# Optimization experiments

Hardware: AMD Instinct MI355X
Metric: run time of the kernel (lower is better)

## Reference

```python
import jax, jax.numpy as jnp
import numpy as np

# Model dims (Gemma-class)
B, T, HID = 1, 3072, 2048
H, KH, D = 16, 8, 128          # q heads, kv heads, head_dim
WIN = 1024                     # sliding window
EPS = 1e-6
SEQ = 1536                     # two packed sequences of length 1536


def _rms(x, w):
    # torch nn.RMSNorm: x * rsqrt(mean(x^2) + eps) [* weight]
    var = jnp.mean(x * x, axis=-1, keepdims=True)
    y = x * jax.lax.rsqrt(var + EPS)
    return y if w is None else y * w


def _rotate_half(x):
    x1, x2 = jnp.split(x, 2, axis=-1)
    return jnp.concatenate([-x2, x1], axis=-1)


def _rope(x, cos, sin):
    # x: [B,T,h,D]; cos/sin: [B,T,rd] -> unsqueeze head dim (matches cos.unsqueeze(2))
    c = cos[:, :, None, :]
    s = sin[:, :, None, :]
    rd = cos.shape[-1]
    xr, xp = x[..., :rd], x[..., rd:]
    xr = xr * c + _rotate_half(xr) * s
    return jnp.concatenate([xr, xp], axis=-1)


def _build_mask(cu_seqlens):
    # causal & within sliding window & same packed sequence (matches _sliding_mask)
    idx = jnp.arange(T)
    seg = jnp.searchsorted(cu_seqlens, idx, side='right') - 1
    i = idx[:, None]
    j = idx[None, :]
    return (i >= j) & ((i - j) < WIN) & (seg[:, None] == seg[None, :])


def _attn_layer(x, wq, qn, k, v, wo, cos, sin, mask):
    # x: [B,T,HID]; k,v: [T,KH,D] (possibly shared from an earlier layer)
    q = _rope(_rms((x @ wq).reshape(B, T, H, D), qn), cos, sin).reshape(T, H, D)
    rep = H // k.shape[1]
    kk = jnp.repeat(k, rep, axis=1)   # GQA: repeat_interleave over head dim
    vv = jnp.repeat(v, rep, axis=1)
    s = jnp.einsum('qhd,khd->hqk', q, kk)          # scale = 1.0 (as in source)
    s = jnp.where(mask, s, jnp.asarray(-1e30, s.dtype))
    p = jax.nn.softmax(s, axis=-1)
    o = jnp.einsum('hqk,khd->qhd', p, vv).reshape(B, T, H * D)
    return o @ wo


def setup_inputs() -> dict:
    key = jax.random.key(0)
    ks = jax.random.split(key, 10)
    hidden_states = jax.random.normal(ks[0], (B, T, HID), jnp.float32)
    # RoPE tables with per-packed-sequence position resets
    pos = jnp.concatenate([jnp.arange(SEQ), jnp.arange(SEQ)]).astype(jnp.float32)
    inv = 1.0 / (10000.0 ** (jnp.arange(0, D, 2, dtype=jnp.float32) / D))
    fr = pos[:, None] * inv[None, :]
    emb = jnp.concatenate([fr, fr], axis=-1)     # [T, D]
    cos = jnp.cos(emb)[None]                     # [1, T, D]
    sin = jnp.sin(emb)[None]
    w = lambda k, sh: 0.02 * jax.random.normal(k, sh, jnp.float32)
    return {
        'hidden_states': hidden_states,
        'cos': cos, 'sin': sin,
        'wq0': w(ks[1], (HID, H * D)), 'wk0': w(ks[2], (HID, KH * D)),
        'wv0': w(ks[3], (HID, KH * D)), 'wo0': w(ks[4], (H * D, HID)),
        'qn0': 1.0 + 0.01 * jax.random.normal(ks[5], (D,), jnp.float32),
        'kn0': 1.0 + 0.01 * jax.random.normal(ks[6], (D,), jnp.float32),
        'wq1': w(ks[7], (HID, H * D)), 'wo1': w(ks[8], (H * D, HID)),
        'qn1': 1.0 + 0.01 * jax.random.normal(ks[9], (D,), jnp.float32),
        'cu_seqlens': jnp.array([0, SEQ, T], dtype=jnp.int32),
    }


def reference(hidden_states, cos, sin, wq0, wk0, wv0, wo0, qn0, kn0, wq1, wo1, qn1, cu_seqlens):
    mask = _build_mask(cu_seqlens)
    # Layer 0: source layer -> computes and stores K/V
    k = _rope(_rms((hidden_states @ wk0).reshape(B, T, KH, D), kn0), cos, sin).reshape(T, KH, D)
    v = _rms((hidden_states @ wv0).reshape(B, T, KH, D), None).reshape(T, KH, D)
    out0 = _attn_layer(hidden_states, wq0, qn0, k, v, wo0, cos, sin, mask)
    # Layer 1: KV-shared layer -> reuses layer 0's K/V (skips k/v projections)
    out1 = _attn_layer(out0, wq1, qn1, k, v, wo1, cos, sin, mask)
    return out1
```

## Files before the change

### kernel.cpp

```cpp
#include <hip/hip_runtime.h>
#include <hip/hip_bf16.h>

#define T_TOK 3072
#define HIDDEN 2048
#define NHQ 16
#define NHKV 8
#define DH 128
#define WINDOW 1024

typedef __attribute__((ext_vector_type(4))) float f32x4;
typedef __attribute__((ext_vector_type(8))) short bf16x8;
typedef __attribute__((ext_vector_type(8))) unsigned short ushort8;
typedef __attribute__((ext_vector_type(4))) unsigned short ushort4v;

__device__ __forceinline__ unsigned short f2bf(float f) {
  union { float fv; unsigned u; } v; v.fv = f;
  unsigned r = v.u + 0x7fffu + ((v.u >> 16) & 1u);
  return (unsigned short)(r >> 16);
}
__device__ __forceinline__ float bf2f(unsigned short h) {
  union { unsigned u; float f; } v; v.u = ((unsigned)h) << 16;
  return v.f;
}
__device__ __forceinline__ void split2(float f, unsigned short& hi, unsigned short& lo) {
  hi = f2bf(f);
  lo = f2bf(f - bf2f(hi));
}

__global__ __launch_bounds__(256) void cvt_split(const float* __restrict__ x,
                                                 unsigned short* __restrict__ yh,
                                                 unsigned short* __restrict__ yl, int n) {
  int i = (blockIdx.x * 256 + threadIdx.x) * 4;
  if (i >= n) return;
  f32x4 v = *(const f32x4*)(x + i);
  ushort4v oh, ol;
#pragma unroll
  for (int j = 0; j < 4; ++j) {
    unsigned short h, l;
    split2(v[j], h, l);
    oh[j] = h; ol[j] = l;
  }
  *(ushort4v*)(yh + i) = oh;
  *(ushort4v*)(yl + i) = ol;
}

__global__ __launch_bounds__(256) void transpose_w_split(const float* __restrict__ W,
                                                         unsigned short* __restrict__ Wth,
                                                         unsigned short* __restrict__ Wtl,
                                                         int K, int N) {
  __shared__ float tile[32][33];
  int bn = blockIdx.x * 32, bk = blockIdx.y * 32;
  int tx = threadIdx.x & 31, ty = threadIdx.x >> 5;
#pragma unroll
  for (int i = 0; i < 4; ++i)
    tile[ty + i * 8][tx] = W[(size_t)(bk + ty + i * 8) * N + bn + tx];
  __syncthreads();
#pragma unroll
  for (int i = 0; i < 4; ++i) {
    unsigned short h, l;
    split2(tile[tx][ty + i * 8], h, l);
    Wth[(size_t)(bn + ty + i * 8) * K + bk + tx] = h;
    if (Wtl) Wtl[(size_t)(bn + ty + i * 8) * K + bk + tx] = l;
  }
}

__global__ __launch_bounds__(256) void transpose_u16(const unsigned short* __restrict__ src,
                                                     unsigned short* __restrict__ dst,
                                                     int R, int C) {
  __shared__ unsigned short tile[32][33];
  int bc = blockIdx.x * 32, br = blockIdx.y * 32;
  int tx = threadIdx.x & 31, ty = threadIdx.x >> 5;
#pragma unroll
  for (int i = 0; i < 4; ++i)
    tile[ty + i * 8][tx] = src[(size_t)(br + ty + i * 8) * C + bc + tx];
  __syncthreads();
#pragma unroll
  for (int i = 0; i < 4; ++i)
    dst[(size_t)(bc + ty + i * 8) * R + br + tx] = tile[tx][ty + i * 8];
}

__global__ __launch_bounds__(256) void gemm3_128(const unsigned short* __restrict__ Ah,
                                                 const unsigned short* __restrict__ Al,
                                                 const unsigned short* __restrict__ Bh,
                                                 const unsigned short* __restrict__ Bl,
                                                 float* __restrict__ Cq,
                                                 float* __restrict__ Ckv,
                                                 int strd, int M, int N, int K) {
  __shared__ unsigned short ah_lds[128 * 32];
  __shared__ unsigned short al_lds[128 * 32];
  __shared__ unsigned short bh_lds[128 * 32];
  __shared__ unsigned short bl_lds[128 * 32];
  const int tid = threadIdx.x, lane = tid & 63, wave = tid >> 6;
  const int wr = (wave >> 1) * 64, wc = (wave & 1) * 64;
  const int g = lane >> 4, r16 = lane & 15;
  int nwg = gridDim.x * gridDim.y;
  int id = blockIdx.y * gridDim.x + blockIdx.x;
  int nid = (id & 7) * (nwg >> 3) + (id >> 3);
  const int bm = nid % gridDim.x, bn = nid / gridDim.x;
  f32x4 acc[4][4];
#pragma unroll
  for (int i = 0; i < 4; ++i)
#pragma unroll
    for (int j = 0; j < 4; ++j) acc[i][j] = (f32x4){0.f, 0.f, 0.f, 0.f};

  const unsigned short* AhB = Ah + (size_t)bm * 128 * K;
  const unsigned short* AlB = Al + (size_t)bm * 128 * K;
  const unsigned short* BhB = Bh + (size_t)bn * 128 * K;
  const unsigned short* BlB = Bl + (size_t)bn * 128 * K;

  for (int kt = 0; kt < K; kt += 32) {
    __syncthreads();
#pragma unroll
    for (int c = 0; c < 2; ++c) {
      size_t goff = (size_t)(wave * 32 + c * 16 + (lane >> 2)) * K + kt + (lane & 3) * 8;
      int loff = (wave * 2 + c) * 512;
      __builtin_amdgcn_global_load_lds(
          (const __attribute__((address_space(1))) unsigned int*)(AhB + goff),
          (__attribute__((address_space(3))) unsigned int*)(ah_lds + loff), 16, 0, 0);
      __builtin_amdgcn_global_load_lds(
          (const __attribute__((address_space(1))) unsigned int*)(AlB + goff),
          (__attribute__((address_space(3))) unsigned int*)(al_lds + loff), 16, 0, 0);
      __builtin_amdgcn_global_load_lds(
          (const __attribute__((address_space(1))) unsigned int*)(BhB + goff),
          (__attribute__((address_space(3))) unsigned int*)(bh_lds + loff), 16, 0, 0);
      __builtin_amdgcn_global_load_lds(
          (const __attribute__((address_space(1))) unsigned int*)(BlB + goff),
          (__attribute__((address_space(3))) unsigned int*)(bl_lds + loff), 16, 0, 0);
    }
    __syncthreads();
    bf16x8 ahf[4], alf[4], bhf[4], blf[4];
#pragma unroll
    for (int i = 0; i < 4; ++i) {
      ahf[i] = *(const bf16x8*)&ah_lds[(wr + i * 16 + r16) * 32 + g * 8];
      alf[i] = *(const bf16x8*)&al_lds[(wr + i * 16 + r16) * 32 + g * 8];
      bhf[i] = *(const bf16x8*)&bh_lds[(wc + i * 16 + r16) * 32 + g * 8];
      blf[i] = *(const bf16x8*)&bl_lds[(wc + i * 16 + r16) * 32 + g * 8];
    }
#pragma unroll
    for (int i = 0; i < 4; ++i)
#pragma unroll
      for (int j = 0; j < 4; ++j) {
        acc[i][j] = __builtin_amdgcn_mfma_f32_16x16x32_bf16(ahf[i], bhf[j], acc[i][j], 0, 0, 0);
        acc[i][j] = __builtin_amdgcn_mfma_f32_16x16x32_bf16(ahf[i], blf[j], acc[i][j], 0, 0, 0);
        acc[i][j] = __builtin_amdgcn_mfma_f32_16x16x32_bf16(alf[i], bhf[j], acc[i][j], 0, 0, 0);
      }
  }

#pragma unroll
  for (int i = 0; i < 4; ++i) {
    int row = bm * 128 + wr + i * 16 + g * 4;
#pragma unroll
    for (int j = 0; j < 4; ++j) {
      int colg = bn * 128 + wc + j * 16 + r16;
      float* Cb; int cc;
      if (colg < 2048) { Cb = Cq; cc = colg; } else { Cb = Ckv; cc = colg - 2048; }
#pragma unroll
      for (int r = 0; r < 4; ++r)
        Cb[(size_t)(row + r) * strd + cc] = acc[i][j][r];
    }
  }
}

template <int OUT>
__global__ __launch_bounds__(256) void gemm3_96(const unsigned short* __restrict__ Ah,
                                                const unsigned short* __restrict__ Al,
                                                const unsigned short* __restrict__ Bh,
                                                const unsigned short* __restrict__ Bl,
                                                float* __restrict__ Cf,
                                                unsigned short* __restrict__ Ch,
                                                unsigned short* __restrict__ Cl,
                                                int M, int N, int K) {
  __shared__ unsigned short ah_lds[96 * 32];
  __shared__ unsigned short al_lds[96 * 32];
  __shared__ unsigned short bh_lds[128 * 32];
  __shared__ unsigned short bl_lds[128 * 32];
  const int tid = threadIdx.x, lane = tid & 63, wave = tid >> 6;
  const int wr = (wave >> 1) * 48, wc = (wave & 1) * 64;
  const int g = lane >> 4, r16 = lane & 15;
  int nwg = gridDim.x * gridDim.y;
  int id = blockIdx.y * gridDim.x + blockIdx.x;
  int nid = (id & 7) * (nwg >> 3) + (id >> 3);
  const int bm = nid % gridDim.x, bn = nid / gridDim.x;
  f32x4 acc[3][4];
#pragma unroll
  for (int i = 0; i < 3; ++i)
#pragma unroll
    for (int j = 0; j < 4; ++j) acc[i][j] = (f32x4){0.f, 0.f, 0.f, 0.f};

  const unsigned short* AhB = Ah + (size_t)bm * 96 * K;
  const unsigned short* AlB = Al + (size_t)bm * 96 * K;
  const unsigned short* BhB = Bh + (size_t)bn * 128 * K;
  const unsigned short* BlB = Bl + (size_t)bn * 128 * K;

  for (int kt = 0; kt < K; kt += 32) {
    __syncthreads();
    {
      int c = wave;
      size_t goff = (size_t)(c * 16 + (lane >> 2)) * K + kt + (lane & 3) * 8;
      __builtin_amdgcn_global_load_lds(
          (const __attribute__((address_space(1))) unsigned int*)(AhB + goff),
          (__attribute__((address_space(3))) unsigned int*)(ah_lds + c * 512), 16, 0, 0);
      __builtin_amdgcn_global_load_lds(
          (const __attribute__((address_space(1))) unsigned int*)(AlB + goff),
          (__attribute__((address_space(3))) unsigned int*)(al_lds + c * 512), 16, 0, 0);
      if (wave < 2) {
        int c2 = 4 + wave;
        size_t goff2 = (size_t)(c2 * 16 + (lane >> 2)) * K + kt + (lane & 3) * 8;
        __builtin_amdgcn_global_load_lds(
            (const __attribute__((address_space(1))) unsigned int*)(AhB + goff2),
            (__attribute__((address_space(3))) unsigned int*)(ah_lds + c2 * 512), 16, 0, 0);
        __builtin_amdgcn_global_load_lds(
            (const __attribute__((address_space(1))) unsigned int*)(AlB + goff2),
            (__attribute__((address_space(3))) unsigned int*)(al_lds + c2 * 512), 16, 0, 0);
      }
    }
#pragma unroll
    for (int c = 0; c < 2; ++c) {
      size_t goff = (size_t)(wave * 32 + c * 16 + (lane >> 2)) * K + kt + (lane & 3) * 8;
      int loff = (wave * 2 + c) * 512;
      __builtin_amdgcn_global_load_lds(
          (const __attribute__((address_space(1))) unsigned int*)(BhB + goff),
          (__attribute__((address_space(3))) unsigned int*)(bh_lds + loff), 16, 0, 0);
      __builtin_amdgcn_global_load_lds(
          (const __attribute__((address_space(1))) unsigned int*)(BlB + goff),
          (__attribute__((address_space(3))) unsigned int*)(bl_lds + loff), 16, 0, 0);
    }
    __syncthreads();
    bf16x8 ahf[3], alf[3], bhf[4], blf[4];
#pragma unroll
    for (int i = 0; i < 3; ++i) {
      ahf[i] = *(const bf16x8*)&ah_lds[(wr + i * 16 + r16) * 32 + g * 8];
      alf[i] = *(const bf16x8*)&al_lds[(wr + i * 16 + r16) * 32 + g * 8];
    }
#pragma unroll
    for (int j = 0; j < 4; ++j) {
      bhf[j] = *(const bf16x8*)&bh_lds[(wc + j * 16 + r16) * 32 + g * 8];
      blf[j] = *(const bf16x8*)&bl_lds[(wc + j * 16 + r16) * 32 + g * 8];
    }
#pragma unroll
    for (int i = 0; i < 3; ++i)
#pragma unroll
      for (int j = 0; j < 4; ++j) {
        acc[i][j] = __builtin_amdgcn_mfma_f32_16x16x32_bf16(ahf[i], bhf[j], acc[i][j], 0, 0, 0);
        acc[i][j] = __builtin_amdgcn_mfma_f32_16x16x32_bf16(ahf[i], blf[j], acc[i][j], 0, 0, 0);
        acc[i][j] = __builtin_amdgcn_mfma_f32_16x16x32_bf16(alf[i], bhf[j], acc[i][j], 0, 0, 0);
      }
  }

#pragma unroll
  for (int i = 0; i < 3; ++i) {
    int row = bm * 96 + wr + i * 16 + g * 4;
#pragma unroll
    for (int j = 0; j < 4; ++j) {
      int col = bn * 128 + wc + j * 16 + r16;
#pragma unroll
      for (int r = 0; r < 4; ++r) {
        if (OUT == 0) {
          Cf[(size_t)(row + r) * N + col] = acc[i][j][r];
        } else {
          unsigned short h, l;
          split2(acc[i][j][r], h, l);
          Ch[(size_t)(row + r) * N + col] = h;
          Cl[(size_t)(row + r) * N + col] = l;
        }
      }
    }
  }
}

__global__ __launch_bounds__(256) void gemm1_96(const unsigned short* __restrict__ Ah,
                                                const unsigned short* __restrict__ Bh,
                                                float* __restrict__ Cf,
                                                int M, int N, int K) {
  __shared__ unsigned short ah_lds[96 * 32];
  __shared__ unsigned short bh_lds[128 * 32];
  const int tid = threadIdx.x, lane = tid & 63, wave = tid >> 6;
  const int wr = (wave >> 1) * 48, wc = (wave & 1) * 64;
  const int g = lane >> 4, r16 = lane & 15;
  int nwg = gridDim.x * gridDim.y;
  int id = blockIdx.y * gridDim.x + blockIdx.x;
  int nid = (id & 7) * (nwg >> 3) + (id >> 3);
  const int bm = nid % gridDim.x, bn = nid / gridDim.x;
  f32x4 acc[3][4];
#pragma unroll
  for (int i = 0; i < 3; ++i)
#pragma unroll
    for (int j = 0; j < 4; ++j) acc[i][j] = (f32x4){0.f, 0.f, 0.f, 0.f};

  const unsigned short* AhB = Ah + (size_t)bm * 96 * K;
  const unsigned short* BhB = Bh + (size_t)bn * 128 * K;

  for (int kt = 0; kt < K; kt += 32) {
    __syncthreads();
    {
      int c = wave;
      size_t goff = (size_t)(c * 16 + (lane >> 2)) * K + kt + (lane & 3) * 8;
      __builtin_amdgcn_global_load_lds(
          (const __attribute__((address_space(1))) unsigned int*)(AhB + goff),
          (__attribute__((address_space(3))) unsigned int*)(ah_lds + c * 512), 16, 0, 0);
      if (wave < 2) {
        int c2 = 4 + wave;
        size_t goff2 = (size_t)(c2 * 16 + (lane >> 2)) * K + kt + (lane & 3) * 8;
        __builtin_amdgcn_global_load_lds(
            (const __attribute__((address_space(1))) unsigned int*)(AhB + goff2),
            (__attribute__((address_space(3))) unsigned int*)(ah_lds + c2 * 512), 16, 0, 0);
      }
    }
#pragma unroll
    for (int c = 0; c < 2; ++c) {
      size_t goff = (size_t)(wave * 32 + c * 16 + (lane >> 2)) * K + kt + (lane & 3) * 8;
      __builtin_amdgcn_global_load_lds(
          (const __attribute__((address_space(1))) unsigned int*)(BhB + goff),
          (__attribute__((address_space(3))) unsigned int*)(bh_lds + (wave * 2 + c) * 512), 16, 0, 0);
    }
    __syncthreads();
    bf16x8 ahf[3], bhf[4];
#pragma unroll
    for (int i = 0; i < 3; ++i)
      ahf[i] = *(const bf16x8*)&ah_lds[(wr + i * 16 + r16) * 32 + g * 8];
#pragma unroll
    for (int j = 0; j < 4; ++j)
      bhf[j] = *(const bf16x8*)&bh_lds[(wc + j * 16 + r16) * 32 + g * 8];
#pragma unroll
    for (int i = 0; i < 3; ++i)
#pragma unroll
      for (int j = 0; j < 4; ++j)
        acc[i][j] = __builtin_amdgcn_mfma_f32_16x16x32_bf16(ahf[i], bhf[j], acc[i][j], 0, 0, 0);
  }

#pragma unroll
  for (int i = 0; i < 3; ++i) {
    int row = bm * 96 + wr + i * 16 + g * 4;
#pragma unroll
    for (int j = 0; j < 4; ++j) {
      int col = bn * 128 + wc + j * 16 + r16;
#pragma unroll
      for (int r = 0; r < 4; ++r)
        Cf[(size_t)(row + r) * N + col] = acc[i][j][r];
    }
  }
}

__global__ __launch_bounds__(256) void rms_rope_split(const float* __restrict__ X,
                                                      const float* __restrict__ w,
                                                      const float* __restrict__ cosp,
                                                      const float* __restrict__ sinp,
                                                      unsigned short* __restrict__ outh,
                                                      unsigned short* __restrict__ outl,
                                                      int NH, int doRope, int XS, int XO) {
  int row = blockIdx.x * 4 + (threadIdx.x >> 6);
  int lane = threadIdx.x & 63;
  int t = row / NH, hh_ = row % NH;
  const float* x = X + (size_t)t * XS + XO + (size_t)hh_ * DH;
  float x1 = x[lane], x2 = x[lane + 64];
  float ss = x1 * x1 + x2 * x2;
#pragma unroll
  for (int m = 1; m < 64; m <<= 1) ss += __shfl_xor(ss, m, 64);
  float inv = rsqrtf(ss * (1.0f / 128.0f) + 1e-6f);
  float y1 = x1 * inv, y2 = x2 * inv;
  if (w) { y1 *= w[lane]; y2 *= w[lane + 64]; }
  if (doRope) {
    float c1 = cosp[t * DH + lane], s1 = sinp[t * DH + lane];
    float c2 = cosp[t * DH + lane + 64], s2 = sinp[t * DH + lane + 64];
    float o1 = y1 * c1 - y2 * s1;
    float o2 = y2 * c2 + y1 * s2;
    y1 = o1; y2 = o2;
  }
  unsigned short h, l;
  split2(y1, h, l);
  outh[(size_t)row * DH + lane] = h;
  if (outl) outl[(size_t)row * DH + lane] = l;
  split2(y2, h, l);
  outh[(size_t)row * DH + lane + 64] = h;
  if (outl) outl[(size_t)row * DH + lane + 64] = l;
}

template <int WRITE_LO>
__global__ __launch_bounds__(256) void attn3(const unsigned short* __restrict__ Qh,
                                             const unsigned short* __restrict__ Ql,
                                             const unsigned short* __restrict__ Kh,
                                             const unsigned short* __restrict__ Kl,
                                             const unsigned short* __restrict__ Vth,
                                             unsigned short* __restrict__ Oh,
                                             unsigned short* __restrict__ Ol,
                                             const int* __restrict__ cu, int ncu) {
  __shared__ unsigned short kh_lds[32][136];
  __shared__ unsigned short kl_lds[32][136];
  __shared__ unsigned short vh_lds[144][40];
  __shared__ unsigned short ph_lds[4][16][44];

  int id = blockIdx.y * gridDim.x + blockIdx.x;
  int nid = (id & 7) * 96 + (id >> 3);
  const int qt = nid % 48, h = nid / 48;
  const int qbase = qt * 64;
  const int kvh = h >> 1;
  const int tid = threadIdx.x, lane = tid & 63, wave = tid >> 6;
  const int g = lane >> 4, r16 = lane & 15;

  for (int i = tid; i < 16 * 40; i += 256) {
    int rr = i / 40, cc = i % 40;
    vh_lds[128 + rr][cc] = (rr == 0) ? (unsigned short)0x3F80 : (unsigned short)0;
  }

  bf16x8 aqh[4], aql[4];
  {
    const size_t qoff = ((size_t)(qbase + wave * 16 + r16) * NHQ + h) * DH;
#pragma unroll
    for (int ks = 0; ks < 4; ++ks) {
      aqh[ks] = *(const bf16x8*)(Qh + qoff + ks * 32 + g * 8);
      aql[ks] = *(const bf16x8*)(Ql + qoff + ks * 32 + g * 8);
    }
  }

  int ssr[4];
#pragma unroll
  for (int r = 0; r < 4; ++r) {
    int q_r = qbase + wave * 16 + g * 4 + r;
    int s = 0;
    for (int i = 1; i < ncu; ++i) { int v = cu[i]; if (v <= q_r) s = v; }
    ssr[r] = s;
  }
  int ss_base = 0;
  for (int i = 1; i < ncu; ++i) { int v = cu[i]; if (v <= qbase) ss_base = v; }

  float m_r[4] = {-1e30f, -1e30f, -1e30f, -1e30f};
  f32x4 oacc[8];
#pragma unroll
  for (int db = 0; db < 8; ++db) oacc[db] = (f32x4){0.f, 0.f, 0.f, 0.f};
  f32x4 oaccL = (f32x4){0.f, 0.f, 0.f, 0.f};

  int lo = qbase - WINDOW + 1;
  if (lo < ss_base) lo = ss_base;
  if (lo < 0) lo = 0;
  int kt0 = lo & ~31;
  int ktend = qbase + 63;

  const int krow = tid >> 3, kc = tid & 7;
  const int vd = tid >> 1, vhalf = (tid & 1) * 16;
  const int qmin = qbase + wave * 16;
  const int sw0 = ((kc + (krow & 15)) & 15) * 16;
  const int sw1 = ((kc + 8 + (krow & 15)) & 15) * 16;

  ushort8 rkh0, rkh1, rkl0, rkl1, rvh0, rvh1;
  auto loadTile = [&](int kt) {
    size_t goff = ((size_t)(kt + krow) * NHKV + kvh) * DH + kc * 8;
    rkh0 = *(const ushort8*)(Kh + goff);
    rkh1 = *(const ushort8*)(Kh + goff + 64);
    rkl0 = *(const ushort8*)(Kl + goff);
    rkl1 = *(const ushort8*)(Kl + goff + 64);
    size_t voff = ((size_t)kvh * DH + vd) * T_TOK + kt + vhalf;
    rvh0 = *(const ushort8*)(Vth + voff);
    rvh1 = *(const ushort8*)(Vth + voff + 8);
  };
  auto writeTile = [&]() {
    char* kbh = (char*)&kh_lds[krow][0];
    char* kbl = (char*)&kl_lds[krow][0];
    *(ushort8*)(kbh + sw0) = rkh0;
    *(ushort8*)(kbh + sw1) = rkh1;
    *(ushort8*)(kbl + sw0) = rkl0;
    *(ushort8*)(kbl + sw1) = rkl1;
    *(ushort8*)&vh_lds[vd][vhalf] = rvh0;
    *(ushort8*)&vh_lds[vd][vhalf + 8] = rvh1;
  };

  loadTile(kt0);
  writeTile();
  __syncthreads();

  for (int kt = kt0; kt <= ktend; kt += 32) {
    const bool hasNext = (kt + 32 <= ktend);
    if (hasNext) loadTile(kt + 32);

    f32x4 s0 = (f32x4){0.f, 0.f, 0.f, 0.f}, s1 = (f32x4){0.f, 0.f, 0.f, 0.f};
    {
      const char* kb0h = (const char*)&kh_lds[r16][0];
      const char* kb1h = (const char*)&kh_lds[16 + r16][0];
      const char* kb0l = (const char*)&kl_lds[r16][0];
      const char* kb1l = (const char*)&kl_lds[16 + r16][0];
#pragma unroll
      for (int ks = 0; ks < 4; ++ks) {
        int sl = ((ks * 4 + g + r16) & 15) * 16;
        bf16x8 bh0 = *(const bf16x8*)(kb0h + sl);
        bf16x8 bh1 = *(const bf16x8*)(kb1h + sl);
        bf16x8 bl0 = *(const bf16x8*)(kb0l + sl);
        bf16x8 bl1 = *(const bf16x8*)(kb1l + sl);
        s0 = __builtin_amdgcn_mfma_f32_16x16x32_bf16(aqh[ks], bh0, s0, 0, 0, 0);
        s0 = __builtin_amdgcn_mfma_f32_16x16x32_bf16(aqh[ks], bl0, s0, 0, 0, 0);
        s0 = __builtin_amdgcn_mfma_f32_16x16x32_bf16(aql[ks], bh0, s0, 0, 0, 0);
        s1 = __builtin_amdgcn_mfma_f32_16x16x32_bf16(aqh[ks], bh1, s1, 0, 0, 0);
        s1 = __builtin_amdgcn_mfma_f32_16x16x32_bf16(aqh[ks], bl1, s1, 0, 0, 0);
        s1 = __builtin_amdgcn_mfma_f32_16x16x32_bf16(aql[ks], bh1, s1, 0, 0, 0);
      }
    }

    float sv0_[4], sv1_[4], mt_[4];
    bool ok0_[4], ok1_[4];
    bool interior = (kt + 31 <= qmin) && (kt >= qmin + 16 - WINDOW) &&
                    __all(kt >= ssr[3]);
    if (interior) {
#pragma unroll
      for (int r = 0; r < 4; ++r) {
        ok0_[r] = ok1_[r] = true;
        sv0_[r] = s0[r]; sv1_[r] = s1[r];
      }
    } else {
#pragma unroll
      for (int r = 0; r < 4; ++r) {
        int q_r = qmin + g * 4 + r;
        int k0 = kt + r16, k1 = k0 + 16;
        ok0_[r] = (k0 <= q_r) && (k0 > q_r - WINDOW) && (k0 >= ssr[r]);
        ok1_[r] = (k1 <= q_r) && (k1 > q_r - WINDOW) && (k1 >= ssr[r]);
        sv0_[r] = ok0_[r] ? s0[r] : -1e30f;
        sv1_[r] = ok1_[r] ? s1[r] : -1e30f;
      }
    }
#pragma unroll
    for (int r = 0; r < 4; ++r) {
      float mt = fmaxf(sv0_[r], sv1_[r]);
#pragma unroll
      for (int mm = 1; mm < 16; mm <<= 1) mt = fmaxf(mt, __shfl_xor(mt, mm, 64));
      mt_[r] = mt;
    }
    float grow = fmaxf(fmaxf(mt_[0] - m_r[0], mt_[1] - m_r[1]),
                       fmaxf(mt_[2] - m_r[2], mt_[3] - m_r[3]));
    if (!__all(grow <= 8.0f)) {
#pragma unroll
      for (int r = 0; r < 4; ++r) {
        float mnew = fmaxf(m_r[r], mt_[r]);
        float alpha = __expf(m_r[r] - mnew);
        m_r[r] = mnew;
#pragma unroll
        for (int db = 0; db < 8; ++db) oacc[db][r] *= alpha;
        oaccL[r] *= alpha;
      }
    }
#pragma unroll
    for (int r = 0; r < 4; ++r) {
      float p0v = ok0_[r] ? __expf(sv0_[r] - m_r[r]) : 0.f;
      float p1v = ok1_[r] ? __expf(sv1_[r] - m_r[r]) : 0.f;
      ph_lds[wave][g * 4 + r][r16] = f2bf(p0v);
      ph_lds[wave][g * 4 + r][16 + r16] = f2bf(p1v);
    }

    bf16x8 pah = *(const bf16x8*)&ph_lds[wave][r16][g * 8];
#pragma unroll
    for (int db = 0; db < 8; ++db) {
      bf16x8 vfh = *(const bf16x8*)&vh_lds[db * 16 + r16][g * 8];
      oacc[db] = __builtin_amdgcn_mfma_f32_16x16x32_bf16(pah, vfh, oacc[db], 0, 0, 0);
    }
    {
      bf16x8 vfo = *(const bf16x8*)&vh_lds[128 + r16][g * 8];
      oaccL = __builtin_amdgcn_mfma_f32_16x16x32_bf16(pah, vfo, oaccL, 0, 0, 0);
    }

    __syncthreads();
    if (hasNext) writeTile();
    __syncthreads();
  }

#pragma unroll
  for (int r = 0; r < 4; ++r) {
    int q_r = qbase + wave * 16 + g * 4 + r;
    float lsum = __shfl(oaccL[r], lane & 48, 64);
    float invl = 1.f / lsum;
#pragma unroll
    for (int db = 0; db < 8; ++db) {
      float ov = oacc[db][r] * invl;
      unsigned short hh, ll;
      split2(ov, hh, ll);
      Oh[(size_t)q_r * (NHQ * DH) + h * DH + db * 16 + r16] = hh;
      if (WRITE_LO) Ol[(size_t)q_r * (NHQ * DH) + h * DH + db * 16 + r16] = ll;
    }
  }
}

extern "C" void kernel_launch(void* const* d_in, const int* in_sizes, int n_in,
                              void* d_out, int out_size, void* d_ws, size_t ws_size,
                              hipStream_t stream) {
  const float* hidden = (const float*)d_in[0];
  const float* cosp   = (const float*)d_in[1];
  const float* sinp   = (const float*)d_in[2];
  const float* wq0    = (const float*)d_in[3];
  const float* wk0    = (const float*)d_in[4];
  const float* wv0    = (const float*)d_in[5];
  const float* wo0    = (const float*)d_in[6];
  const float* qn0    = (const float*)d_in[7];
  const float* kn0    = (const float*)d_in[8];
  const float* wq1    = (const float*)d_in[9];
  const float* wo1    = (const float*)d_in[10];
  const float* qn1    = (const float*)d_in[11];
  const int*   cu     = (const int*)d_in[12];
  int ncu = in_sizes[12];
  (void)n_in; (void)out_size;

  const int nX = T_TOK * HIDDEN;
  const int KVN = NHKV * DH;

  char* p = (char*)d_ws;
  auto alloc = [&](size_t bytes) { char* r = p; p += (bytes + 255) & ~255ull; return r; };

  const size_t NEED_FUSED = 173ull * 1024 * 1024;
  bool fusedOK = (ws_size >= NEED_FUSED);

  if (fusedOK) {
    float*          c32q  = (float*)alloc((size_t)T_TOK * HIDDEN * 4);
    float*          c32kv = (float*)alloc((size_t)T_TOK * HIDDEN * 4);
    unsigned short* xh    = (unsigned short*)alloc((size_t)T_TOK * HIDDEN * 2);
    unsigned short* xl    = (unsigned short*)alloc((size_t)T_TOK * HIDDEN * 2);
    unsigned short* wth   = (unsigned short*)alloc((size_t)2 * HIDDEN * HIDDEN * 2);
    unsigned short* wtl   = (unsigned short*)alloc((size_t)2 * HIDDEN * HIDDEN * 2);
    unsigned short* qh    = (unsigned short*)alloc((size_t)T_TOK * NHQ * DH * 2);
    unsigned short* ql    = (unsigned short*)alloc((size_t)T_TOK * NHQ * DH * 2);
    unsigned short* kh    = (unsigned short*)alloc((size_t)T_TOK * KVN * 2);
    unsigned short* kl    = (unsigned short*)alloc((size_t)T_TOK * KVN * 2);
    unsigned short* x1h   = (unsigned short*)alloc((size_t)T_TOK * HIDDEN * 2);
    unsigned short* x1l   = (unsigned short*)alloc((size_t)T_TOK * HIDDEN * 2);
    unsigned short* vh    = (unsigned short*)c32q;
    unsigned short* vth   = vh + (size_t)T_TOK * KVN;

    cvt_split<<<nX / 1024, 256, 0, stream>>>(hidden, xh, xl, nX);

    transpose_w_split<<<dim3(HIDDEN / 32, HIDDEN / 32), 256, 0, stream>>>(wq0, wth, wtl, HIDDEN, HIDDEN);
    transpose_w_split<<<dim3(KVN / 32, HIDDEN / 32), 256, 0, stream>>>(
        wk0, wth + (size_t)HIDDEN * HIDDEN, wtl + (size_t)HIDDEN * HIDDEN, HIDDEN, KVN);
    transpose_w_split<<<dim3(KVN / 32, HIDDEN / 32), 256, 0, stream>>>(
        wv0, wth + (size_t)(HIDDEN + KVN) * HIDDEN, wtl + (size_t)(HIDDEN + KVN) * HIDDEN, HIDDEN, KVN);

    gemm3_128<<<dim3(T_TOK / 128, 4096 / 128), 256, 0, stream>>>(
        xh, xl, wth, wtl, c32q, c32kv, HIDDEN, T_TOK, 4096, HIDDEN);

    rms_rope_split<<<T_TOK * NHQ / 4, 256, 0, stream>>>(c32q, qn0, cosp, sinp, qh, ql, NHQ, 1, HIDDEN, 0);
    rms_rope_split<<<T_TOK * NHKV / 4, 256, 0, stream>>>(c32kv, kn0, cosp, sinp, kh, kl, NHKV, 1, HIDDEN, 0);
    rms_rope_split<<<T_TOK * NHKV / 4, 256, 0, stream>>>(c32kv, nullptr, cosp, sinp, vh, nullptr, NHKV, 0, HIDDEN, KVN);

    transpose_u16<<<dim3(KVN / 32, T_TOK / 32), 256, 0, stream>>>(vh, vth, T_TOK, KVN);

    attn3<1><<<dim3(T_TOK / 64, NHQ), 256, 0, stream>>>(qh, ql, kh, kl, vth, xh, xl, cu, ncu);

    transpose_w_split<<<dim3(HIDDEN / 32, HIDDEN / 32), 256, 0, stream>>>(wo0, wth, wtl, HIDDEN, HIDDEN);
    gemm3_96<2><<<dim3(T_TOK / 96, HIDDEN / 128), 256, 0, stream>>>(
        xh, xl, wth, wtl, nullptr, x1h, x1l, T_TOK, HIDDEN, HIDDEN);

    transpose_w_split<<<dim3(HIDDEN / 32, HIDDEN / 32), 256, 0, stream>>>(wq1, wth, wtl, HIDDEN, HIDDEN);
    gemm3_96<0><<<dim3(T_TOK / 96, HIDDEN / 128), 256, 0, stream>>>(
        x1h, x1l, wth, wtl, c32kv, nullptr, nullptr, T_TOK, HIDDEN, HIDDEN);
    rms_rope_split<<<T_TOK * NHQ / 4, 256, 0, stream>>>(c32kv, qn1, cosp, sinp, qh, ql, NHQ, 1, HIDDEN, 0);

    attn3<0><<<dim3(T_TOK / 64, NHQ), 256, 0, stream>>>(qh, ql, kh, kl, vth, xh, nullptr, cu, ncu);

    transpose_w_split<<<dim3(HIDDEN / 32, HIDDEN / 32), 256, 0, stream>>>(wo1, wth, nullptr, HIDDEN, HIDDEN);
    gemm1_96<<<dim3(T_TOK / 96, HIDDEN / 128), 256, 0, stream>>>(xh, wth, (float*)d_out, T_TOK, HIDDEN, HIDDEN);
  } else {
    float*          c32  = (float*)alloc((size_t)T_TOK * HIDDEN * 4);
    unsigned short* xh   = (unsigned short*)alloc((size_t)T_TOK * HIDDEN * 2);
    unsigned short* xl   = (unsigned short*)alloc((size_t)T_TOK * HIDDEN * 2);
    unsigned short* wth  = (unsigned short*)alloc((size_t)HIDDEN * HIDDEN * 2);
    unsigned short* wtl  = (unsigned short*)alloc((size_t)HIDDEN * HIDDEN * 2);
    unsigned short* qh   = (unsigned short*)alloc((size_t)T_TOK * NHQ * DH * 2);
    unsigned short* ql   = (unsigned short*)alloc((size_t)T_TOK * NHQ * DH * 2);
    unsigned short* kh   = (unsigned short*)alloc((size_t)T_TOK * KVN * 2);
    unsigned short* kl   = (unsigned short*)alloc((size_t)T_TOK * KVN * 2);
    unsigned short* vh   = (unsigned short*)alloc((size_t)T_TOK * KVN * 2);
    unsigned short* vth  = (unsigned short*)alloc((size_t)T_TOK * KVN * 2);
    unsigned short* x1h  = (unsigned short*)alloc((size_t)T_TOK * HIDDEN * 2);
    unsigned short* x1l  = (unsigned short*)alloc((size_t)T_TOK * HIDDEN * 2);

    cvt_split<<<nX / 1024, 256, 0, stream>>>(hidden, xh, xl, nX);

    transpose_w_split<<<dim3(HIDDEN / 32, HIDDEN / 32), 256, 0, stream>>>(wq0, wth, wtl, HIDDEN, HIDDEN);
    gemm3_128<<<dim3(T_TOK / 128, HIDDEN / 128), 256, 0, stream>>>(
        xh, xl, wth, wtl, c32, c32, HIDDEN, T_TOK, HIDDEN, HIDDEN);
    rms_rope_split<<<T_TOK * NHQ / 4, 256, 0, stream>>>(c32, qn0, cosp, sinp, qh, ql, NHQ, 1, HIDDEN, 0);

    transpose_w_split<<<dim3(KVN / 32, HIDDEN / 32), 256, 0, stream>>>(wk0, wth, wtl, HIDDEN, KVN);
    gemm3_128<<<dim3(T_TOK / 128, KVN / 128), 256, 0, stream>>>(
        xh, xl, wth, wtl, c32, c32, KVN, T_TOK, KVN, HIDDEN);
    rms_rope_split<<<T_TOK * NHKV / 4, 256, 0, stream>>>(c32, kn0, cosp, sinp, kh, kl, NHKV, 1, KVN, 0);

    transpose_w_split<<<dim3(KVN / 32, HIDDEN / 32), 256, 0, stream>>>(wv0, wth, wtl, HIDDEN, KVN);
    gemm3_128<<<dim3(T_TOK / 128, KVN / 128), 256, 0, stream>>>(
        xh, xl, wth, wtl, c32, c32, KVN, T_TOK, KVN, HIDDEN);
    rms_rope_split<<<T_TOK * NHKV / 4, 256, 0, stream>>>(c32, nullptr, cosp, sinp, vh, nullptr, NHKV, 0, KVN, 0);

    transpose_u16<<<dim3(KVN / 32, T_TOK / 32), 256, 0, stream>>>(vh, vth, T_TOK, KVN);

    attn3<1><<<dim3(T_TOK / 64, NHQ), 256, 0, stream>>>(qh, ql, kh, kl, vth, xh, xl, cu, ncu);

    transpose_w_split<<<dim3(HIDDEN / 32, HIDDEN / 32), 256, 0, stream>>>(wo0, wth, wtl, HIDDEN, HIDDEN);
    gemm3_96<2><<<dim3(T_TOK / 96, HIDDEN / 128), 256, 0, stream>>>(
        xh, xl, wth, wtl, nullptr, x1h, x1l, T_TOK, HIDDEN, HIDDEN);

    transpose_w_split<<<dim3(HIDDEN / 32, HIDDEN / 32), 256, 0, stream>>>(wq1, wth, wtl, HIDDEN, HIDDEN);
    gemm3_96<0><<<dim3(T_TOK / 96, HIDDEN / 128), 256, 0, stream>>>(
        x1h, x1l, wth, wtl, c32, nullptr, nullptr, T_TOK, HIDDEN, HIDDEN);
    rms_rope_split<<<T_TOK * NHQ / 4, 256, 0, stream>>>(c32, qn1, cosp, sinp, qh, ql, NHQ, 1, HIDDEN, 0);

    attn3<0><<<dim3(T_TOK / 64, NHQ), 256, 0, stream>>>(qh, ql, kh, kl, vth, xh, nullptr, cu, ncu);

    transpose_w_split<<<dim3(HIDDEN / 32, HIDDEN / 32), 256, 0, stream>>>(wo1, wth, nullptr, HIDDEN, HIDDEN);
    gemm1_96<<<dim3(T_TOK / 96, HIDDEN / 128), 256, 0, stream>>>(xh, wth, (float*)d_out, T_TOK, HIDDEN, HIDDEN);
  }
}
```

Before: 676.2 us.

## Fuse Q RMSNorm and RoPE into attention, widen query tile to 96 rows

The attention kernel now reads the fp32 Q projection directly. Each wave applies the RMSNorm, weight and RoPE in registers and splits the result into hi/lo bf16, so the separate rms_rope_split launches and the qh/ql round trips through memory go away. Each block now covers 96 query rows with 6 waves (384 threads), with only the first 256 threads staging K/V tiles, so each staged K/V tile is reused by more queries. The workspace-size fallback path is removed and the fused path is always taken. In exchange, fp32 Q reads are larger and strided by HIDDEN, the block has fewer blocks overall, and there is more register pressure.

```diff
diff --git a/kernel.cpp b/kernel.cpp
--- a/kernel.cpp
+++ b/kernel.cpp
@@ -376,8 +376,10 @@
 }
 
 template <int WRITE_LO>
-__global__ __launch_bounds__(256) void attn3(const unsigned short* __restrict__ Qh,
-                                             const unsigned short* __restrict__ Ql,
+__global__ __launch_bounds__(384) void attn3(const float* __restrict__ Qf,
+                                             const float* __restrict__ qnw,
+                                             const float* __restrict__ cosp,
+                                             const float* __restrict__ sinp,
                                              const unsigned short* __restrict__ Kh,
                                              const unsigned short* __restrict__ Kl,
                                              const unsigned short* __restrict__ Vth,
@@ -387,28 +389,72 @@
   __shared__ unsigned short kh_lds[32][136];
   __shared__ unsigned short kl_lds[32][136];
   __shared__ unsigned short vh_lds[144][40];
-  __shared__ unsigned short ph_lds[4][16][44];
+  __shared__ unsigned short ph_lds[6][16][44];
 
   int id = blockIdx.y * gridDim.x + blockIdx.x;
-  int nid = (id & 7) * 96 + (id >> 3);
-  const int qt = nid % 48, h = nid / 48;
-  const int qbase = qt * 64;
+  int nid = (id & 7) * 64 + (id >> 3);
+  const int qt = nid & 31, h = nid >> 5;
+  const int qbase = qt * 96;
   const int kvh = h >> 1;
   const int tid = threadIdx.x, lane = tid & 63, wave = tid >> 6;
   const int g = lane >> 4, r16 = lane & 15;
 
-  for (int i = tid; i < 16 * 40; i += 256) {
+  for (int i = tid; i < 16 * 40; i += 384) {
     int rr = i / 40, cc = i % 40;
     vh_lds[128 + rr][cc] = (rr == 0) ? (unsigned short)0x3F80 : (unsigned short)0;
   }
 
   bf16x8 aqh[4], aql[4];
   {
-    const size_t qoff = ((size_t)(qbase + wave * 16 + r16) * NHQ + h) * DH;
+    int q_r = qbase + wave * 16 + r16;
+    const float* xq = Qf + (size_t)q_r * HIDDEN + h * DH;
+    float xv[4][8];
+    float ss = 0.f;
 #pragma unroll
     for (int ks = 0; ks < 4; ++ks) {
-      aqh[ks] = *(const bf16x8*)(Qh + qoff + ks * 32 + g * 8);
-      aql[ks] = *(const bf16x8*)(Ql + qoff + ks * 32 + g * 8);
+      f32x4 a = *(const f32x4*)(xq + ks * 32 + g * 8);
+      f32x4 b = *(const f32x4*)(xq + ks * 32 + g * 8 + 4);
+#pragma unroll
+      for (int j = 0; j < 4; ++j) { xv[ks][j] = a[j]; xv[ks][4 + j] = b[j]; }
+#pragma unroll
+      for (int j = 0; j < 8; ++j) ss += xv[ks][j] * xv[ks][j];
+    }
+    ss += __shfl_xor(ss, 16, 64);
+    ss += __shfl_xor(ss, 32, 64);
+    float inv = rsqrtf(ss * (1.0f / 128.0f) + 1e-6f);
+    float y[4][8];
+#pragma unroll
+    for (int ks = 0; ks < 4; ++ks) {
+      f32x4 w0 = *(const f32x4*)(qnw + ks * 32 + g * 8);
+      f32x4 w1 = *(const f32x4*)(qnw + ks * 32 + g * 8 + 4);
+#pragma unroll
+      for (int j = 0; j < 4; ++j) {
+        y[ks][j] = xv[ks][j] * inv * w0[j];
+        y[ks][4 + j] = xv[ks][4 + j] * inv * w1[j];
+      }
+    }
+    const float* cb = cosp + (size_t)q_r * DH;
+    const float* sb = sinp + (size_t)q_r * DH;
+#pragma unroll
+    for (int ks = 0; ks < 4; ++ks) {
+      bf16x8 th, tl;
+#pragma unroll
+      for (int j2 = 0; j2 < 2; ++j2) {
+        int col = ks * 32 + g * 8 + j2 * 4;
+        f32x4 cv = *(const f32x4*)(cb + col);
+        f32x4 sv = *(const f32x4*)(sb + col);
+#pragma unroll
+        for (int j = 0; j < 4; ++j) {
+          float o;
+          if (ks < 2) o = y[ks][j2 * 4 + j] * cv[j] - y[ks + 2][j2 * 4 + j] * sv[j];
+          else        o = y[ks][j2 * 4 + j] * cv[j] + y[ks - 2][j2 * 4 + j] * sv[j];
+          unsigned short hx, lx;
+          split2(o, hx, lx);
+          th[j2 * 4 + j] = (short)hx;
+          tl[j2 * 4 + j] = (short)lx;
+        }
+      }
+      aqh[ks] = th; aql[ks] = tl;
     }
   }
 
@@ -433,16 +479,18 @@
   if (lo < ss_base) lo = ss_base;
   if (lo < 0) lo = 0;
   int kt0 = lo & ~31;
-  int ktend = qbase + 63;
-
-  const int krow = tid >> 3, kc = tid & 7;
-  const int vd = tid >> 1, vhalf = (tid & 1) * 16;
+  int ktend = qbase + 95;
+
+  const bool stager = tid < 256;
+  const int krow = (tid & 255) >> 3, kc = tid & 7;
+  const int vd = (tid & 255) >> 1, vhalf = (tid & 1) * 16;
   const int qmin = qbase + wave * 16;
   const int sw0 = ((kc + (krow & 15)) & 15) * 16;
   const int sw1 = ((kc + 8 + (krow & 15)) & 15) * 16;
 
   ushort8 rkh0, rkh1, rkl0, rkl1, rvh0, rvh1;
   auto loadTile = [&](int kt) {
+    if (!stager) return;
     size_t goff = ((size_t)(kt + krow) * NHKV + kvh) * DH + kc * 8;
     rkh0 = *(const ushort8*)(Kh + goff);
     rkh1 = *(const ushort8*)(Kh + goff + 64);
@@ -453,6 +501,7 @@
     rvh1 = *(const ushort8*)(Vth + voff + 8);
   };
   auto writeTile = [&]() {
+    if (!stager) return;
     char* kbh = (char*)&kh_lds[krow][0];
     char* kbl = (char*)&kl_lds[krow][0];
     *(ushort8*)(kbh + sw0) = rkh0;
@@ -591,7 +640,7 @@
   const float* qn1    = (const float*)d_in[11];
   const int*   cu     = (const int*)d_in[12];
   int ncu = in_sizes[12];
-  (void)n_in; (void)out_size;
+  (void)n_in; (void)out_size; (void)ws_size;
 
   const int nX = T_TOK * HIDDEN;
   const int KVN = NHKV * DH;
@@ -599,105 +648,47 @@
   char* p = (char*)d_ws;
   auto alloc = [&](size_t bytes) { char* r = p; p += (bytes + 255) & ~255ull; return r; };
 
-  const size_t NEED_FUSED = 173ull * 1024 * 1024;
-  bool fusedOK = (ws_size >= NEED_FUSED);
-
-  if (fusedOK) {
-    float*          c32q  = (float*)alloc((size_t)T_TOK * HIDDEN * 4);
-    float*          c32kv = (float*)alloc((size_t)T_TOK * HIDDEN * 4);
-    unsigned short* xh    = (unsigned short*)alloc((size_t)T_TOK * HIDDEN * 2);
-    unsigned short* xl    = (unsigned short*)alloc((size_t)T_TOK * HIDDEN * 2);
-    unsigned short* wth   = (unsigned short*)alloc((size_t)2 * HIDDEN * HIDDEN * 2);
-    unsigned short* wtl   = (unsigned short*)alloc((size_t)2 * HIDDEN * HIDDEN * 2);
-    unsigned short* qh    = (unsigned short*)alloc((size_t)T_TOK * NHQ * DH * 2);
-    unsigned short* ql    = (unsigned short*)alloc((size_t)T_TOK * NHQ * DH * 2);
-    unsigned short* kh    = (unsigned short*)alloc((size_t)T_TOK * KVN * 2);
-    unsigned short* kl    = (unsigned short*)alloc((size_t)T_TOK * KVN * 2);
-    unsigned short* x1h   = (unsigned short*)alloc((size_t)T_TOK * HIDDEN * 2);
-    unsigned short* x1l   = (unsigned short*)alloc((size_t)T_TOK * HIDDEN * 2);
-    unsigned short* vh    = (unsigned short*)c32q;
-    unsigned short* vth   = vh + (size_t)T_TOK * KVN;
-
-    cvt_split<<<nX / 1024, 256, 0, stream>>>(hidden, xh, xl, nX);
-
-    transpose_w_split<<<dim3(HIDDEN / 32, HIDDEN / 32), 256, 0, stream>>>(wq0, wth, wtl, HIDDEN, HIDDEN);
-    transpose_w_split<<<dim3(KVN / 32, HIDDEN / 32), 256, 0, stream>>>(
-        wk0, wth + (size_t)HIDDEN * HIDDEN, wtl + (size_t)HIDDEN * HIDDEN, HIDDEN, KVN);
-    transpose_w_split<<<dim3(KVN / 32, HIDDEN / 32), 256, 0, stream>>>(
-        wv0, wth + (size_t)(HIDDEN + KVN) * HIDDEN, wtl + (size_t)(HIDDEN + KVN) * HIDDEN, HIDDEN, KVN);
-
-    gemm3_128<<<dim3(T_TOK / 128, 4096 / 128), 256, 0, stream>>>(
-        xh, xl, wth, wtl, c32q, c32kv, HIDDEN, T_TOK, 4096, HIDDEN);
-
-    rms_rope_split<<<T_TOK * NHQ / 4, 256, 0, stream>>>(c32q, qn0, cosp, sinp, qh, ql, NHQ, 1, HIDDEN, 0);
-    rms_rope_split<<<T_TOK * NHKV / 4, 256, 0, stream>>>(c32kv, kn0, cosp, sinp, kh, kl, NHKV, 1, HIDDEN, 0);
-    rms_rope_split<<<T_TOK * NHKV / 4, 256, 0, stream>>>(c32kv, nullptr, cosp, sinp, vh, nullptr, NHKV, 0, HIDDEN, KVN);
-
-    transpose_u16<<<dim3(KVN / 32, T_TOK / 32), 256, 0, stream>>>(vh, vth, T_TOK, KVN);
-
-    attn3<1><<<dim3(T_TOK / 64, NHQ), 256, 0, stream>>>(qh, ql, kh, kl, vth, xh, xl, cu, ncu);
-
-    transpose_w_split<<<dim3(HIDDEN / 32, HIDDEN / 32), 256, 0, stream>>>(wo0, wth, wtl, HIDDEN, HIDDEN);
-    gemm3_96<2><<<dim3(T_TOK / 96, HIDDEN / 128), 256, 0, stream>>>(
-        xh, xl, wth, wtl, nullptr, x1h, x1l, T_TOK, HIDDEN, HIDDEN);
-
-    transpose_w_split<<<dim3(HIDDEN / 32, HIDDEN / 32), 256, 0, stream>>>(wq1, wth, wtl, HIDDEN, HIDDEN);
-    gemm3_96<0><<<dim3(T_TOK / 96, HIDDEN / 128), 256, 0, stream>>>(
-        x1h, x1l, wth, wtl, c32kv, nullptr, nullptr, T_TOK, HIDDEN, HIDDEN);
-    rms_rope_split<<<T_TOK * NHQ / 4, 256, 0, stream>>>(c32kv, qn1, cosp, sinp, qh, ql, NHQ, 1, HIDDEN, 0);
-
-    attn3<0><<<dim3(T_TOK / 64, NHQ), 256, 0, stream>>>(qh, ql, kh, kl, vth, xh, nullptr, cu, ncu);
-
-    transpose_w_split<<<dim3(HIDDEN / 32, HIDDEN / 32), 256, 0, stream>>>(wo1, wth, nullptr, HIDDEN, HIDDEN);
-    gemm1_96<<<dim3(T_TOK / 96, HIDDEN / 128), 256, 0, stream>>>(xh, wth, (float*)d_out, T_TOK, HIDDEN, HIDDEN);
-  } else {
-    float*          c32  = (float*)alloc((size_t)T_TOK * HIDDEN * 4);
-    unsigned short* xh   = (unsigned short*)alloc((size_t)T_TOK * HIDDEN * 2);
-    unsigned short* xl   = (unsigned short*)alloc((size_t)T_TOK * HIDDEN * 2);
-    unsigned short* wth  = (unsigned short*)alloc((size_t)HIDDEN * HIDDEN * 2);
-    unsigned short* wtl  = (unsigned short*)alloc((size_t)HIDDEN * HIDDEN * 2);
-    unsigned short* qh   = (unsigned short*)alloc((size_t)T_TOK * NHQ * DH * 2);
-    unsigned short* ql   = (unsigned short*)alloc((size_t)T_TOK * NHQ * DH * 2);
-    unsigned short* kh   = (unsigned short*)alloc((size_t)T_TOK * KVN * 2);
-    unsigned short* kl   = (unsigned short*)alloc((size_t)T_TOK * KVN * 2);
-    unsigned short* vh   = (unsigned short*)alloc((size_t)T_TOK * KVN * 2);
-    unsigned short* vth  = (unsigned short*)alloc((size_t)T_TOK * KVN * 2);
-    unsigned short* x1h  = (unsigned short*)alloc((size_t)T_TOK * HIDDEN * 2);
-    unsigned short* x1l  = (unsigned short*)alloc((size_t)T_TOK * HIDDEN * 2);
-
-    cvt_split<<<nX / 1024, 256, 0, stream>>>(hidden, xh, xl, nX);
-
-    transpose_w_split<<<dim3(HIDDEN / 32, HIDDEN / 32), 256, 0, stream>>>(wq0, wth, wtl, HIDDEN, HIDDEN);
-    gemm3_128<<<dim3(T_TOK / 128, HIDDEN / 128), 256, 0, stream>>>(
-        xh, xl, wth, wtl, c32, c32, HIDDEN, T_TOK, HIDDEN, HIDDEN);
-    rms_rope_split<<<T_TOK * NHQ / 4, 256, 0, stream>>>(c32, qn0, cosp, sinp, qh, ql, NHQ, 1, HIDDEN, 0);
-
-    transpose_w_split<<<dim3(KVN / 32, HIDDEN / 32), 256, 0, stream>>>(wk0, wth, wtl, HIDDEN, KVN);
-    gemm3_128<<<dim3(T_TOK / 128, KVN / 128), 256, 0, stream>>>(
-        xh, xl, wth, wtl, c32, c32, KVN, T_TOK, KVN, HIDDEN);
-    rms_rope_split<<<T_TOK * NHKV / 4, 256, 0, stream>>>(c32, kn0, cosp, sinp, kh, kl, NHKV, 1, KVN, 0);
-
-    transpose_w_split<<<dim3(KVN / 32, HIDDEN / 32), 256, 0, stream>>>(wv0, wth, wtl, HIDDEN, KVN);
-    gemm3_128<<<dim3(T_TOK / 128, KVN / 128), 256, 0, stream>>>(
-        xh, xl, wth, wtl, c32, c32, KVN, T_TOK, KVN, HIDDEN);
-    rms_rope_split<<<T_TOK * NHKV / 4, 256, 0, stream>>>(c32, nullptr, cosp, sinp, vh, nullptr, NHKV, 0, KVN, 0);
-
-    transpose_u16<<<dim3(KVN / 32, T_TOK / 32), 256, 0, stream>>>(vh, vth, T_TOK, KVN);
-
-    attn3<1><<<dim3(T_TOK / 64, NHQ), 256, 0, stream>>>(qh, ql, kh, kl, vth, xh, xl, cu, ncu);
-
-    transpose_w_split<<<dim3(HIDDEN / 32, HIDDEN / 32), 256, 0, stream>>>(wo0, wth, wtl, HIDDEN, HIDDEN);
-    gemm3_96<2><<<dim3(T_TOK / 96, HIDDEN / 128), 256, 0, stream>>>(
-        xh, xl, wth, wtl, nullptr, x1h, x1l, T_TOK, HIDDEN, HIDDEN);
-
-    transpose_w_split<<<dim3(HIDDEN / 32, HIDDEN / 32), 256, 0, stream>>>(wq1, wth, wtl, HIDDEN, HIDDEN);
-    gemm3_96<0><<<dim3(T_TOK / 96, HIDDEN / 128), 256, 0, stream>>>(
-        x1h, x1l, wth, wtl, c32, nullptr, nullptr, T_TOK, HIDDEN, HIDDEN);
-    rms_rope_split<<<T_TOK * NHQ / 4, 256, 0, stream>>>(c32, qn1, cosp, sinp, qh, ql, NHQ, 1, HIDDEN, 0);
-
-    attn3<0><<<dim3(T_TOK / 64, NHQ), 256, 0, stream>>>(qh, ql, kh, kl, vth, xh, nullptr, cu, ncu);
-
-    transpose_w_split<<<dim3(HIDDEN / 32, HIDDEN / 32), 256, 0, stream>>>(wo1, wth, nullptr, HIDDEN, HIDDEN);
-    gemm1_96<<<dim3(T_TOK / 96, HIDDEN / 128), 256, 0, stream>>>(xh, wth, (float*)d_out, T_TOK, HIDDEN, HIDDEN);
-  }
-}
+  float*          c32q  = (float*)alloc((size_t)T_TOK * HIDDEN * 4);
+  float*          c32kv = (float*)alloc((size_t)T_TOK * HIDDEN * 4);
+  unsigned short* xh    = (unsigned short*)alloc((size_t)T_TOK * HIDDEN * 2);
+  unsigned short* xl    = (unsigned short*)alloc((size_t)T_TOK * HIDDEN * 2);
+  unsigned short* wth   = (unsigned short*)alloc((size_t)2 * HIDDEN * HIDDEN * 2);
+  unsigned short* wtl   = (unsigned short*)alloc((size_t)2 * HIDDEN * HIDDEN * 2);
+  unsigned short* kh    = (unsigned short*)alloc((size_t)T_TOK * KVN * 2);
+  unsigned short* kl    = (unsigned short*)alloc((size_t)T_TOK * KVN * 2);
+  unsigned short* vh    = (unsigned short*)alloc((size_t)T_TOK * KVN * 2);
+  unsigned short* vth   = (unsigned short*)alloc((size_t)T_TOK * KVN * 2);
+  unsigned short* x1h   = (unsigned short*)alloc((size_t)T_TOK * HIDDEN * 2);
+  unsigned short* x1l   = (unsigned short*)alloc((size_t)T_TOK * HIDDEN * 2);
+
+  cvt_split<<<nX / 1024, 256, 0, stream>>>(hidden, xh, xl, nX);
+
+  transpose_w_split<<<dim3(HIDDEN / 32, HIDDEN / 32), 256, 0, stream>>>(wq0, wth, wtl, HIDDEN, HIDDEN);
+  transpose_w_split<<<dim3(KVN / 32, HIDDEN / 32), 256, 0, stream>>>(
+      wk0, wth + (size_t)HIDDEN * HIDDEN, wtl + (size_t)HIDDEN * HIDDEN, HIDDEN, KVN);
+  transpose_w_split<<<dim3(KVN / 32, HIDDEN / 32), 256, 0, stream>>>(
+      wv0, wth + (size_t)(HIDDEN + KVN) * HIDDEN, wtl + (size_t)(HIDDEN + KVN) * HIDDEN, HIDDEN, KVN);
+
+  gemm3_128<<<dim3(T_TOK / 128, 4096 / 128), 256, 0, stream>>>(
+      xh, xl, wth, wtl, c32q, c32kv, HIDDEN, T_TOK, 4096, HIDDEN);
+
+  rms_rope_split<<<T_TOK * NHKV / 4, 256, 0, stream>>>(c32kv, kn0, cosp, sinp, kh, kl, NHKV, 1, HIDDEN, 0);
+  rms_rope_split<<<T_TOK * NHKV / 4, 256, 0, stream>>>(c32kv, nullptr, cosp, sinp, vh, nullptr, NHKV, 0, HIDDEN, KVN);
+
+  transpose_u16<<<dim3(KVN / 32, T_TOK / 32), 256, 0, stream>>>(vh, vth, T_TOK, KVN);
+
+  attn3<1><<<dim3(32, 16), 384, 0, stream>>>(c32q, qn0, cosp, sinp, kh, kl, vth, xh, xl, cu, ncu);
+
+  transpose_w_split<<<dim3(HIDDEN / 32, HIDDEN / 32), 256, 0, stream>>>(wo0, wth, wtl, HIDDEN, HIDDEN);
+  gemm3_96<2><<<dim3(T_TOK / 96, HIDDEN / 128), 256, 0, stream>>>(
+      xh, xl, wth, wtl, nullptr, x1h, x1l, T_TOK, HIDDEN, HIDDEN);
+
+  transpose_w_split<<<dim3(HIDDEN / 32, HIDDEN / 32), 256, 0, stream>>>(wq1, wth, wtl, HIDDEN, HIDDEN);
+  gemm3_96<0><<<dim3(T_TOK / 96, HIDDEN / 128), 256, 0, stream>>>(
+      x1h, x1l, wth, wtl, c32kv, nullptr, nullptr, T_TOK, HIDDEN, HIDDEN);
+
+  attn3<0><<<dim3(32, 16), 384, 0, stream>>>(c32kv, qn1, cosp, sinp, kh, kl, vth, xh, nullptr, cu, ncu);
+
+  transpose_w_split<<<dim3(HIDDEN / 32, HIDDEN / 32), 256, 0, stream>>>(wo1, wth, nullptr, HIDDEN, HIDDEN);
+  gemm1_96<<<dim3(T_TOK / 96, HIDDEN / 128), 256, 0, stream>>>(xh, wth, (float*)d_out, T_TOK, HIDDEN, HIDDEN);
+}
```

Result: no change. 678.7 us (+0.4%).
